# Performance work log

Measured on AMD Instinct MI355X. Metric: run time of the kernel, lower is better.

The kernel has to match this reference:

```python
import jax, jax.numpy as jnp
import numpy as np

# ---- static config (mirrors PaCoVoxelLoss init) ----
NUM_QUERIES = 20
FACTOR = 64
NUM_GT = 12
K_NEIGHBORS = 8          # repulsion.num_neighbors
REP_EPS = 1e-12          # repulsion.epsilon
BANDWIDTH = 0.03         # repulsion.kernel_bandwidth
RADIUS = 0.07            # repulsion.radius
ALPHA_PARAM = 0.5
BETA_CHAMFER = 20.0
W_CLS, W_REP, W_CH1, W_CH2 = 1.0, 1.0, 1.0, 1.0
PAD_COST = 1e6           # pad value to square the rectangular assignment problem


def _hungarian(cost):
    # Jonker-Volgenant / e-maxx shortest augmenting path; cost: (n, n) float64.
    # Returns col_to_row: for each column j, the row assigned to it.
    n = cost.shape[0]
    INF = 1e18
    u = np.zeros(n + 1); v = np.zeros(n + 1)
    p = np.zeros(n + 1, dtype=np.int64)
    way = np.zeros(n + 1, dtype=np.int64)
    for i in range(1, n + 1):
        p[0] = i; j0 = 0
        minv = np.full(n + 1, INF)
        used = np.zeros(n + 1, dtype=bool)
        while True:
            used[j0] = True
            i0 = p[j0]; delta = INF; j1 = 0
            for j in range(1, n + 1):
                if not used[j]:
                    cur = cost[i0 - 1, j - 1] - u[i0] - v[j]
                    if cur < minv[j]:
                        minv[j] = cur; way[j] = j0
                    if minv[j] < delta:
                        delta = minv[j]; j1 = j
            for j in range(n + 1):
                if used[j]:
                    u[p[j]] += delta; v[j] -= delta
                else:
                    minv[j] -= delta
            j0 = j1
            if p[j0] == 0:
                break
        while j0 != 0:
            j1 = way[j0]; p[j0] = p[j1]; j0 = j1
    return p[1:] - 1


def _match(cost_np):
    # cost_np: (B, Q, P) with P <= Q -> rows (B, P): pred row matched to each gt col.
    Bn, Qn, Pn = cost_np.shape
    rows = np.zeros((Bn, Pn), dtype=np.int64)
    for b in range(Bn):
        sq = np.full((Qn, Qn), PAD_COST, dtype=np.float64)
        sq[:, :Pn] = cost_np[b].astype(np.float64)
        rows[b] = _hungarian(sq)[:Pn]
    return rows


def _gather_q(A, rows):
    # A: (B, Q, P), rows: (B, P) -> A[b, rows[b,p], p] : (B, P)
    return jnp.take_along_axis(A, rows[:, None, :], axis=1)[:, 0, :]


def _bce_logits(x, t):
    return jnp.maximum(x, 0.0) - x * t + jnp.log1p(jnp.exp(-jnp.abs(x)))


def _cost_terms(pred_normals, pred_distances, gt_normals, gt_distances, points, gt_masks):
    mask_f = gt_masks.astype(points.dtype)           # (B, P, N)
    cnt = mask_f.sum(-1)                             # (B, P)
    # |points . n_q - d_q| for all query planes: (B, Q, N)
    pp = jnp.abs(jnp.einsum('bnd,bqd->bqn', points, pred_normals) - pred_distances[:, :, None])
    cham_raw = jnp.einsum('bqn,bpn->bqp', pp, mask_f) / jnp.maximum(cnt, 1.0)[:, None, :]
    has = (cnt > 0)[:, None, :]                      # (B, 1, P)
    normal_sim = 1.0 - jnp.abs(jnp.einsum('bqd,bpd->bqp', pred_normals, gt_normals))
    dist_diff = jnp.abs(pred_distances[:, :, None] - gt_distances[:, None, :])
    cost = normal_sim + 0.5 * dist_diff + 5.0 * jnp.where(has, cham_raw, 1.0)
    return cost, cham_raw, normal_sim, dist_diff, has


def _losses(pred_logits, pred_normals, pred_distances, gt_normals, gt_distances,
            points, reconstructed_points, gt, gt_masks, rows):
    _, cham_raw, normal_sim, dist_diff, has = _cost_terms(
        pred_normals, pred_distances, gt_normals, gt_distances, points, gt_masks)

    # classification loss: target 1 at matched pred rows
    Qn = pred_logits.shape[1]
    cls_target = jax.nn.one_hot(rows, Qn, dtype=pred_logits.dtype).sum(axis=1)  # (B, Q)
    cls_loss = _bce_logits(pred_logits, cls_target).mean()

    # param loss over matched pairs (mean over P matches, mean over B)
    param_loss = (_gather_q(normal_sim, rows).mean(-1) + _gather_q(dist_diff, rows).mean(-1)).mean()

    # pvd chamfer: point-to-plane term, zero for empty masks, /P /B
    pvd_chamfer = _gather_q(jnp.where(has, cham_raw, 0.0), rows).mean()

    # repulsion loss on per-query point groups
    Bn = reconstructed_points.shape[0]
    rp = reconstructed_points.reshape(Bn, NUM_QUERIES, FACTOR, 3)
    d2 = jnp.sum((rp[:, :, :, None, :] - rp[:, :, None, :, :]) ** 2, axis=-1)  # (B,Q,F,F)
    _, idx = jax.lax.top_k(-d2, K_NEIGHBORS)       # k nearest incl. self
    dn = jnp.maximum(jnp.take_along_axis(d2, idx[..., 1:], axis=-1), REP_EPS)  # (B,Q,F,k-1)
    w = jnp.exp(-dn / BANDWIDTH ** 2)
    rep = jnp.maximum(jnp.mean((RADIUS - jnp.sqrt(dn)) * w, axis=(2, 3)), 0.0).mean()

    # fine-grained chamfer (L1 and L2) between reconstructed and gt clouds
    diff = reconstructed_points[:, :, None, :] - gt[:, None, :, :]  # (B, M, G, 3)
    d1 = jnp.abs(diff).sum(-1)
    d2c = (diff ** 2).sum(-1)
    ch1 = (0.5 * (d1.min(axis=2).mean(axis=1) + d1.min(axis=1).mean(axis=1))).mean()
    ch2 = (0.5 * (d2c.min(axis=2).mean(axis=1) + d2c.min(axis=1).mean(axis=1))).mean()

    total = (W_CLS * cls_loss + ALPHA_PARAM * param_loss + BETA_CHAMFER * pvd_chamfer
             + W_REP * rep + W_CH1 * ch1 + W_CH2 * ch2)
    return total


def setup_inputs() -> dict:
    key = jax.random.key(0)
    ks = jax.random.split(key, 10)
    B, Q, P, N, G = 8, NUM_QUERIES, NUM_GT, 4096, 2048

    def unit(k, shape):
        v = jax.random.normal(k, shape, dtype=jnp.float32)
        return v / jnp.linalg.norm(v, axis=-1, keepdims=True)

    return {
        'pred_logits': jax.random.normal(ks[0], (B, Q), dtype=jnp.float32),
        'pred_normals': unit(ks[1], (B, Q, 3)),
        'pred_distances': jax.random.normal(ks[2], (B, Q), dtype=jnp.float32),
        'gt_normals': unit(ks[3], (B, P, 3)),
        'gt_distances': jax.random.normal(ks[4], (B, P), dtype=jnp.float32),
        'gt_masks': jax.random.bernoulli(ks[5], 0.3, (B, P, N)),
        'points': jax.random.normal(ks[6], (B, N, 3), dtype=jnp.float32),
        'reconstructed_points': 0.5 * jax.random.normal(ks[7], (B, Q * FACTOR, 3), dtype=jnp.float32),
        'gt': jax.random.normal(ks[8], (B, G, 3), dtype=jnp.float32),
        'gt_index': jax.random.randint(ks[9], (B, G), 0, P, dtype=jnp.int64) if jax.config.jax_enable_x64 else jax.random.randint(ks[9], (B, G), 0, P, dtype=jnp.int32),
    }


def reference(pred_logits, pred_normals, pred_distances, gt_normals, gt_distances,
              points, reconstructed_points, gt, gt_masks, gt_index):
    cost = _cost_terms(pred_normals, pred_distances, gt_normals, gt_distances, points, gt_masks)[0]
    rows = jnp.asarray(_match(np.asarray(cost)))  # Hungarian (host, like scipy in original)
    return _losses(pred_logits, pred_normals, pred_distances, gt_normals, gt_distances,
                   points, reconstructed_points, gt, gt_masks, rows)
```

## Files before the change

### kernel.cpp

```cpp
#include <hip/hip_runtime.h>
#include <math.h>

#define Bn 8
#define Qn 20
#define Pn 12
#define Nn 4096
#define Gn 2048
#define Mn 1280
#define Fn 64
#define KNB 7
#define SA 8
#define SB 5


__global__ void mega1_kernel(const float* __restrict__ pred_normals,
                             const float* __restrict__ pred_distances,
                             const float* __restrict__ gt_normals,
                             const float* __restrict__ gt_distances,
                             const float* __restrict__ points,
                             const int*   __restrict__ gt_masks,
                             const float* __restrict__ recon,
                             const float* __restrict__ gt,
                             float* __restrict__ cham, float* __restrict__ ns,
                             float* __restrict__ dd, float* __restrict__ cost,
                             float* __restrict__ cnt, float* __restrict__ acc,
                             float* __restrict__ rep_part,
                             float* __restrict__ pmA1, float* __restrict__ pmA2,
                             float* __restrict__ pmB1, float* __restrict__ pmB2) {
    __shared__ float smem[2 * Pn * 256];
    const int blk = blockIdx.x;
    const int tid = threadIdx.x;

    if (blk < 160) {
        if (blk == 0 && tid < 20) acc[tid] = 0.f;
        const int b = blk / Qn, q = blk % Qn;
        const float nx = pred_normals[(b * Qn + q) * 3 + 0];
        const float ny = pred_normals[(b * Qn + q) * 3 + 1];
        const float nz = pred_normals[(b * Qn + q) * 3 + 2];
        const float dq = pred_distances[b * Qn + q];

        float accs[Pn], accw[Pn];
#pragma unroll
        for (int p = 0; p < Pn; ++p) { accs[p] = 0.f; accw[p] = 0.f; }

        const float* ptb = points + (size_t)b * Nn * 3;
        const int*   mb  = gt_masks + (size_t)b * Pn * Nn;

        for (int n = tid; n < Nn; n += 256) {
            float px = ptb[n * 3 + 0], py = ptb[n * 3 + 1], pz = ptb[n * 3 + 2];
            float pp = fabsf(px * nx + py * ny + pz * nz - dq);
#pragma unroll
            for (int p = 0; p < Pn; ++p) {
                float m = (float)mb[(size_t)p * Nn + n];
                accs[p] += pp * m;
                accw[p] += m;
            }
        }
#pragma unroll
        for (int p = 0; p < Pn; ++p) {
            smem[p * 256 + tid] = accs[p];
            smem[(p + Pn) * 256 + tid] = accw[p];
        }
        __syncthreads();
        for (int off = 128; off > 0; off >>= 1) {
            if (tid < off) {
#pragma unroll
                for (int r = 0; r < 2 * Pn; ++r) smem[r * 256 + tid] += smem[r * 256 + tid + off];
            }
            __syncthreads();
        }
        if (tid < Pn) {
            const int p = tid;
            float c  = smem[(p + Pn) * 256];
            float cv = smem[p * 256] / fmaxf(c, 1.f);
            float gnx = gt_normals[(b * Pn + p) * 3 + 0];
            float gny = gt_normals[(b * Pn + p) * 3 + 1];
            float gnz = gt_normals[(b * Pn + p) * 3 + 2];
            float nsim = 1.f - fabsf(nx * gnx + ny * gny + nz * gnz);
            float ddv  = fabsf(dq - gt_distances[b * Pn + p]);
            int idx = (b * Qn + q) * Pn + p;
            cham[idx] = cv;
            ns[idx]   = nsim;
            dd[idx]   = ddv;
            cost[idx] = nsim + 0.5f * ddv + 5.f * ((c > 0.f) ? cv : 1.f);
            if (q == 0) cnt[b * Pn + p] = c;
        }
    } else if (blk < 200) {
        const int wave = tid >> 6, lane = tid & 63;
        const int g = (blk - 160) * 4 + wave;
        float* xs = smem + wave * 192;
        float* ys = xs + 64;
        float* zs = xs + 128;
        const float* base = recon + (size_t)g * Fn * 3;
        xs[lane] = base[lane * 3 + 0];
        ys[lane] = base[lane * 3 + 1];
        zs[lane] = base[lane * 3 + 2];
        __syncthreads();
        float best[KNB];
#pragma unroll
        for (int k = 0; k < KNB; ++k) best[k] = 3.4e38f;
        const float xi = xs[lane], yi = ys[lane], zi = zs[lane];
        for (int j = 0; j < Fn; ++j) {
            if (j == lane) continue;
            float dx = xi - xs[j], dy = yi - ys[j], dz = zi - zs[j];
            float d2 = dx * dx + dy * dy + dz * dz;
            if (d2 < best[KNB - 1]) {
                int k = KNB - 1;
                while (k > 0 && best[k - 1] > d2) { best[k] = best[k - 1]; --k; }
                best[k] = d2;
            }
        }
        float sum = 0.f;
#pragma unroll
        for (int k = 0; k < KNB; ++k) {
            float dn = fmaxf(best[k], 1e-12f);
            float w  = expf(-dn / (0.03f * 0.03f));
            sum += (0.07f - sqrtf(dn)) * w;
        }
        for (int off = 32; off > 0; off >>= 1) sum += __shfl_down(sum, off);
        if (lane == 0) rep_part[g] = fmaxf(sum / (float)(Fn * KNB), 0.f);
    } else {
        int cblk = blk - 200;
        float* tx = smem;
        float* ty = smem + 256;
        float* tz = smem + 512;
        float x, y, z;
        const float* inner;
        float *o1, *o2;
        int idx;
        if (cblk < 40 * SA) {
            int s = cblk % SA, ob = cblk / SA;
            idx = ob * 256 + tid;
            int b = idx / Mn;
            x = recon[idx * 3 + 0]; y = recon[idx * 3 + 1]; z = recon[idx * 3 + 2];
            inner = gt + ((size_t)b * Gn + s * 256) * 3;
            o1 = pmA1 + s * (Bn * Mn); o2 = pmA2 + s * (Bn * Mn);
        } else {
            cblk -= 40 * SA;
            int s = cblk % SB, ob = cblk / SB;
            idx = ob * 256 + tid;
            int b = idx / Gn;
            x = gt[idx * 3 + 0]; y = gt[idx * 3 + 1]; z = gt[idx * 3 + 2];
            inner = recon + ((size_t)b * Mn + s * 256) * 3;
            o1 = pmB1 + s * (Bn * Gn); o2 = pmB2 + s * (Bn * Gn);
        }
        tx[tid] = inner[tid * 3 + 0];
        ty[tid] = inner[tid * 3 + 1];
        tz[tid] = inner[tid * 3 + 2];
        __syncthreads();
        float m1 = 3.4e38f, m2 = 3.4e38f;
        for (int j = 0; j < 256; ++j) {
            float dx = x - tx[j], dy = y - ty[j], dz = z - tz[j];
            float d1 = fabsf(dx) + fabsf(dy) + fabsf(dz);
            float d2 = dx * dx + dy * dy + dz * dz;
            m1 = fminf(m1, d1); m2 = fminf(m2, d2);
        }
        o1[idx] = m1; o2[idx] = m2;
    }
}

__global__ void hungarian_kernel(const float* __restrict__ cost,
                                 const float* __restrict__ pred_logits,
                                 const float* __restrict__ ns,
                                 const float* __restrict__ dd,
                                 const float* __restrict__ cham,
                                 const float* __restrict__ cnt,
                                 float* __restrict__ acc) {
    const int b = blockIdx.x;
    const int t = threadIdx.x;
    __shared__ double a[Pn * Qn];
    for (int k = t; k < Qn * Pn; k += 64)
        a[(k % Pn) * Qn + (k / Pn)] = (double)cost[b * Qn * Pn + k];
    __syncthreads();

    const int col = t;
    const bool isCol = (col >= 1 && col <= Qn);
    double v = 0.0;
    double u = 0.0;
    double minv = 0.0;
    int way = 0, p = 0;

    for (int i = 1; i <= Pn; ++i) {
        const int p0 = i;
        minv = 1e18;
        bool used = false;
        bool rowInPath = false;
        int j0 = 0;
        while (true) {
            if (col == j0) used = true;
            int i0 = (j0 == 0) ? p0 : __shfl(p, j0);
            if (t == i0) rowInPath = true;
            double u_i0 = __shfl(u, i0);
            double mv = 1e18;
            if (isCol && !used) {
                double cur = a[(i0 - 1) * Qn + (col - 1)] - u_i0 - v;
                if (cur < minv) { minv = cur; way = j0; }
                mv = minv;
            }
            double bv = mv; int bj = col;
#pragma unroll
            for (int off = 16; off > 0; off >>= 1) {
                double ov = __shfl_down(bv, off);
                int    oj = __shfl_down(bj, off);
                if (ov < bv) { bv = ov; bj = oj; }
            }
            double delta = __shfl(bv, 0);
            int    j1    = __shfl(bj, 0);
            if (used || col == 0) v -= delta;
            else if (isCol)       minv -= delta;
            if (rowInPath)        u += delta;
            j0 = j1;
            int pj0 = __shfl(p, j0);
            if (pj0 == 0) break;
        }
        while (j0 != 0) {
            int wj = __shfl(way, j0);
            int pw = (wj == 0) ? p0 : __shfl(p, wj);
            if (col == j0) p = pw;
            j0 = wj;
        }
    }

    float cls = 0.f, par = 0.f, pvd = 0.f;
    if (isCol) {
        float x = pred_logits[b * Qn + (col - 1)];
        float tgt = (p > 0) ? 1.f : 0.f;
        cls = fmaxf(x, 0.f) - x * tgt + log1pf(expf(-fabsf(x)));
        if (p > 0) {
            int idx = (b * Qn + (col - 1)) * Pn + (p - 1);
            par = ns[idx] + dd[idx];
            pvd = (cnt[b * Pn + (p - 1)] > 0.f) ? cham[idx] : 0.f;
        }
    }
    for (int off = 32; off > 0; off >>= 1) {
        cls += __shfl_down(cls, off);
        par += __shfl_down(par, off);
        pvd += __shfl_down(pvd, off);
    }
    if (t == 0) {
        atomicAdd(&acc[0], cls / (float)(Bn * Qn));
        atomicAdd(&acc[1], par / (float)(Bn * Pn));
        atomicAdd(&acc[2], pvd / (float)(Bn * Pn));
    }
}

__global__ void reduce_kernel(const float* __restrict__ pmA1, const float* __restrict__ pmA2,
                              const float* __restrict__ pmB1, const float* __restrict__ pmB2,
                              const float* __restrict__ rep_part,
                              float* __restrict__ acc, int* __restrict__ counter,
                              float* __restrict__ out) {
    const int blk = blockIdx.x;
    const int tid = threadIdx.x;
    float c1 = 0.f, c2 = 0.f;
    if (blk < 40) {
        int idx = blk * 256 + tid;
        float m1 = 3.4e38f, m2 = 3.4e38f;
#pragma unroll
        for (int s = 0; s < SA; ++s) {
            m1 = fminf(m1, pmA1[s * (Bn * Mn) + idx]);
            m2 = fminf(m2, pmA2[s * (Bn * Mn) + idx]);
        }
        c1 = m1 * (0.5f / (float)(Bn * Mn));
        c2 = m2 * (0.5f / (float)(Bn * Mn));
    } else if (blk < 104) {
        int idx = (blk - 40) * 256 + tid;
        float m1 = 3.4e38f, m2 = 3.4e38f;
#pragma unroll
        for (int s = 0; s < SB; ++s) {
            m1 = fminf(m1, pmB1[s * (Bn * Gn) + idx]);
            m2 = fminf(m2, pmB2[s * (Bn * Gn) + idx]);
        }
        c1 = m1 * (0.5f / (float)(Bn * Gn));
        c2 = m2 * (0.5f / (float)(Bn * Gn));
    } else {
        c1 = (tid < Bn * Qn) ? rep_part[tid] / (float)(Bn * Qn) : 0.f;
    }
    __shared__ float s1[256], s2[256];
    s1[tid] = c1; s2[tid] = c2;
    __syncthreads();
    for (int off = 128; off > 0; off >>= 1) {
        if (tid < off) { s1[tid] += s1[tid + off]; s2[tid] += s2[tid + off]; }
        __syncthreads();
    }
    if (tid == 0) {
        if (blk < 104) {
            atomicAdd(&acc[4], s1[0]);
            atomicAdd(&acc[5], s2[0]);
        } else {
            atomicAdd(&acc[3], s1[0]);
        }
        __threadfence();
        int old = atomicAdd(counter, 1);
        if (old == 104) {
            float a0 = atomicAdd(&acc[0], 0.f);
            float a1 = atomicAdd(&acc[1], 0.f);
            float a2 = atomicAdd(&acc[2], 0.f);
            float a3 = atomicAdd(&acc[3], 0.f);
            float a4 = atomicAdd(&acc[4], 0.f);
            float a5 = atomicAdd(&acc[5], 0.f);
            out[0] = a0 + 0.5f * a1 + 20.f * a2 + a3 + a4 + a5;
        }
    }
}

extern "C" void kernel_launch(void* const* d_in, const int* in_sizes, int n_in,
                              void* d_out, int out_size, void* d_ws, size_t ws_size,
                              hipStream_t stream) {
    const float* pred_logits    = (const float*)d_in[0];
    const float* pred_normals   = (const float*)d_in[1];
    const float* pred_distances = (const float*)d_in[2];
    const float* gt_normals     = (const float*)d_in[3];
    const float* gt_distances   = (const float*)d_in[4];
    const int*   gt_masks       = (const int*)d_in[5];
    const float* points         = (const float*)d_in[6];
    const float* recon          = (const float*)d_in[7];
    const float* gt             = (const float*)d_in[8];

    float* ws   = (float*)d_ws;
    float* cham = ws;
    float* ns   = ws + 1920;
    float* dd   = ws + 3840;
    float* cost = ws + 5760;
    float* cnt  = ws + 7680;
    float* acc  = ws + 7872;
    int*   cntr = (int*)(ws + 7888);
    float* rep  = ws + 7904;
    float* pmA1 = ws + 8192;
    float* pmA2 = ws + 90112;
    float* pmB1 = ws + 172032;
    float* pmB2 = ws + 253952;

    mega1_kernel<<<840, 256, 0, stream>>>(pred_normals, pred_distances, gt_normals,
                                          gt_distances, points, gt_masks, recon, gt,
                                          cham, ns, dd, cost, cnt, acc, rep,
                                          pmA1, pmA2, pmB1, pmB2);
    hungarian_kernel<<<Bn, 64, 0, stream>>>(cost, pred_logits, ns, dd, cham, cnt, acc);
    reduce_kernel<<<105, 256, 0, stream>>>(pmA1, pmA2, pmB1, pmB2, rep, acc, cntr,
                                           (float*)d_out);
}
```

Before: 135.4 us.

## Fuse Hungarian and chamfer reduction into main kernel via last-block completion counters

Merges the Hungarian matching kernel and the final reduce kernel into one kernel, adding a small init kernel that zeroes the counters and fills the min buffers with +inf. The last of the 20 cost blocks for each batch runs the Hungarian match. Chamfer partial minima now go through atomicMin on float bits instead of per-slice buffers, and the last slice block for each tile reduces the tile. A global done counter picks which block writes the final output. This removes kernel launch boundaries and intermediate buffer traffic, at the price of atomic writes, counter serialization and a tail that is still serialized.

```diff
diff --git a/kernel.cpp b/kernel.cpp
--- a/kernel.cpp
+++ b/kernel.cpp
@@ -11,28 +11,66 @@
 #define KNB 7
 #define SA 8
 #define SB 5
-
-
-__global__ void mega1_kernel(const float* __restrict__ pred_normals,
-                             const float* __restrict__ pred_distances,
-                             const float* __restrict__ gt_normals,
-                             const float* __restrict__ gt_distances,
-                             const float* __restrict__ points,
-                             const int*   __restrict__ gt_masks,
-                             const float* __restrict__ recon,
-                             const float* __restrict__ gt,
-                             float* __restrict__ cham, float* __restrict__ ns,
-                             float* __restrict__ dd, float* __restrict__ cost,
-                             float* __restrict__ cnt, float* __restrict__ acc,
-                             float* __restrict__ rep_part,
-                             float* __restrict__ pmA1, float* __restrict__ pmA2,
-                             float* __restrict__ pmB1, float* __restrict__ pmB2) {
+#define DONE_TARGET 152
+
+
+__device__ __forceinline__ float aread(float* p) { return atomicAdd(p, 0.0f); }
+__device__ __forceinline__ void awrite(float* p, float v) { atomicExch(p, v); }
+__device__ __forceinline__ unsigned int auread(unsigned int* p) { return atomicAdd(p, 0u); }
+
+__device__ __forceinline__ void contribute(float* acc, int* done, float* out) {
+    __threadfence();
+    int old = atomicAdd(done, 1);
+    if (old == DONE_TARGET - 1) {
+        __threadfence();
+        float a0 = aread(&acc[0]);
+        float a1 = aread(&acc[1]);
+        float a2 = aread(&acc[2]);
+        float a3 = aread(&acc[3]);
+        float a4 = aread(&acc[4]);
+        float a5 = aread(&acc[5]);
+        out[0] = a0 + 0.5f * a1 + 20.f * a2 + a3 + a4 + a5;
+    }
+}
+
+__global__ void init_kernel(unsigned int* wsu) {
+    int tid = blockIdx.x * 256 + threadIdx.x;
+    for (int k = tid; k < 160; k += 64 * 256) wsu[7776 + k] = 0u;
+    for (int k = tid; k < 53248; k += 64 * 256) wsu[8192 + k] = 0x7F800000u;
+}
+
+__global__ void mega_kernel(const float* __restrict__ pred_logits,
+                            const float* __restrict__ pred_normals,
+                            const float* __restrict__ pred_distances,
+                            const float* __restrict__ gt_normals,
+                            const float* __restrict__ gt_distances,
+                            const float* __restrict__ points,
+                            const int*   __restrict__ gt_masks,
+                            const float* __restrict__ recon,
+                            const float* __restrict__ gt,
+                            float* __restrict__ ws, float* __restrict__ out) {
     __shared__ float smem[2 * Pn * 256];
+    __shared__ double hsm[Pn * Qn];
+    __shared__ int sflag;
     const int blk = blockIdx.x;
     const int tid = threadIdx.x;
 
+    float* cham = ws;
+    float* ns   = ws + 1920;
+    float* dd   = ws + 3840;
+    float* cost = ws + 5760;
+    float* cnt  = ws + 7680;
+    float* acc  = ws + 7776;
+    int*   costc  = (int*)(ws + 7784);
+    int*   chamAc = (int*)(ws + 7792);
+    int*   chamBc = (int*)(ws + 7832);
+    int*   done   = (int*)(ws + 7896);
+    unsigned int* mA1u = (unsigned int*)(ws + 8192);
+    unsigned int* mA2u = (unsigned int*)(ws + 18432);
+    unsigned int* mB1u = (unsigned int*)(ws + 28672);
+    unsigned int* mB2u = (unsigned int*)(ws + 45056);
+
     if (blk < 160) {
-        if (blk == 0 && tid < 20) acc[tid] = 0.f;
         const int b = blk / Qn, q = blk % Qn;
         const float nx = pred_normals[(b * Qn + q) * 3 + 0];
         const float ny = pred_normals[(b * Qn + q) * 3 + 1];
@@ -79,11 +117,94 @@
             float nsim = 1.f - fabsf(nx * gnx + ny * gny + nz * gnz);
             float ddv  = fabsf(dq - gt_distances[b * Pn + p]);
             int idx = (b * Qn + q) * Pn + p;
-            cham[idx] = cv;
-            ns[idx]   = nsim;
-            dd[idx]   = ddv;
-            cost[idx] = nsim + 0.5f * ddv + 5.f * ((c > 0.f) ? cv : 1.f);
-            if (q == 0) cnt[b * Pn + p] = c;
+            awrite(&cham[idx], cv);
+            awrite(&ns[idx],   nsim);
+            awrite(&dd[idx],   ddv);
+            awrite(&cost[idx], nsim + 0.5f * ddv + 5.f * ((c > 0.f) ? cv : 1.f));
+            if (q == 0) awrite(&cnt[b * Pn + p], c);
+        }
+        __syncthreads();
+        if (tid == 0) {
+            __threadfence();
+            int old = atomicAdd(&costc[b], 1);
+            sflag = (old == Qn - 1) ? 1 : 0;
+        }
+        __syncthreads();
+        if (!sflag) return;
+        if (tid >= 64) return;
+        __threadfence();
+
+        const int t = tid;
+        for (int k = t; k < Qn * Pn; k += 64)
+            hsm[(k % Pn) * Qn + (k / Pn)] = (double)aread(&cost[b * Qn * Pn + k]);
+
+        const int col = t;
+        const bool isCol = (col >= 1 && col <= Qn);
+        double v = 0.0, u = 0.0, minv = 0.0;
+        int way = 0, p = 0;
+
+        for (int i = 1; i <= Pn; ++i) {
+            const int p0 = i;
+            minv = 1e18;
+            bool used = false;
+            bool rowInPath = false;
+            int j0 = 0;
+            while (true) {
+                if (col == j0) used = true;
+                int i0 = (j0 == 0) ? p0 : __shfl(p, j0);
+                if (t == i0) rowInPath = true;
+                double u_i0 = __shfl(u, i0);
+                double mv = 1e18;
+                if (isCol && !used) {
+                    double cur = hsm[(i0 - 1) * Qn + (col - 1)] - u_i0 - v;
+                    if (cur < minv) { minv = cur; way = j0; }
+                    mv = minv;
+                }
+                double bv = mv; int bj = col;
+#pragma unroll
+                for (int off = 16; off > 0; off >>= 1) {
+                    double ov = __shfl_down(bv, off);
+                    int    oj = __shfl_down(bj, off);
+                    if (ov < bv) { bv = ov; bj = oj; }
+                }
+                double delta = __shfl(bv, 0);
+                int    j1    = __shfl(bj, 0);
+                if (used || col == 0) v -= delta;
+                else if (isCol)       minv -= delta;
+                if (rowInPath)        u += delta;
+                j0 = j1;
+                int pj0 = __shfl(p, j0);
+                if (pj0 == 0) break;
+            }
+            while (j0 != 0) {
+                int wj = __shfl(way, j0);
+                int pw = (wj == 0) ? p0 : __shfl(p, wj);
+                if (col == j0) p = pw;
+                j0 = wj;
+            }
+        }
+
+        float cls = 0.f, par = 0.f, pvd = 0.f;
+        if (isCol) {
+            float x = pred_logits[b * Qn + (col - 1)];
+            float tgt = (p > 0) ? 1.f : 0.f;
+            cls = fmaxf(x, 0.f) - x * tgt + log1pf(expf(-fabsf(x)));
+            if (p > 0) {
+                int idx = (b * Qn + (col - 1)) * Pn + (p - 1);
+                par = aread(&ns[idx]) + aread(&dd[idx]);
+                pvd = (aread(&cnt[b * Pn + (p - 1)]) > 0.f) ? aread(&cham[idx]) : 0.f;
+            }
+        }
+        for (int off = 32; off > 0; off >>= 1) {
+            cls += __shfl_down(cls, off);
+            par += __shfl_down(par, off);
+            pvd += __shfl_down(pvd, off);
+        }
+        if (t == 0) {
+            atomicAdd(&acc[0], cls / (float)(Bn * Qn));
+            atomicAdd(&acc[1], par / (float)(Bn * Pn));
+            atomicAdd(&acc[2], pvd / (float)(Bn * Pn));
+            contribute(acc, done, out);
         }
     } else if (blk < 200) {
         const int wave = tid >> 6, lane = tid & 63;
@@ -95,7 +216,6 @@
         xs[lane] = base[lane * 3 + 0];
         ys[lane] = base[lane * 3 + 1];
         zs[lane] = base[lane * 3 + 2];
-        __syncthreads();
         float best[KNB];
 #pragma unroll
         for (int k = 0; k < KNB; ++k) best[k] = 3.4e38f;
@@ -118,32 +238,40 @@
             sum += (0.07f - sqrtf(dn)) * w;
         }
         for (int off = 32; off > 0; off >>= 1) sum += __shfl_down(sum, off);
-        if (lane == 0) rep_part[g] = fmaxf(sum / (float)(Fn * KNB), 0.f);
+        if (lane == 0) smem[1000 + wave] = fmaxf(sum / (float)(Fn * KNB), 0.f);
+        __syncthreads();
+        if (tid == 0) {
+            float total = (smem[1000] + smem[1001] + smem[1002] + smem[1003]) / (float)(Bn * Qn);
+            atomicAdd(&acc[3], total);
+            contribute(acc, done, out);
+        }
     } else {
-        int cblk = blk - 200;
-        float* tx = smem;
-        float* ty = smem + 256;
-        float* tz = smem + 512;
+        int a = blk - 200;
+        const bool isA = (a < 320);
+        int ob, s, idx;
         float x, y, z;
         const float* inner;
-        float *o1, *o2;
-        int idx;
-        if (cblk < 40 * SA) {
-            int s = cblk % SA, ob = cblk / SA;
+        unsigned int *mu1, *mu2;
+        int* ctr; int target;
+        if (isA) {
+            ob = a / SA; s = a % SA;
             idx = ob * 256 + tid;
             int b = idx / Mn;
             x = recon[idx * 3 + 0]; y = recon[idx * 3 + 1]; z = recon[idx * 3 + 2];
             inner = gt + ((size_t)b * Gn + s * 256) * 3;
-            o1 = pmA1 + s * (Bn * Mn); o2 = pmA2 + s * (Bn * Mn);
+            mu1 = mA1u; mu2 = mA2u; ctr = &chamAc[ob]; target = SA;
         } else {
-            cblk -= 40 * SA;
-            int s = cblk % SB, ob = cblk / SB;
+            a -= 320;
+            ob = a / SB; s = a % SB;
             idx = ob * 256 + tid;
             int b = idx / Gn;
             x = gt[idx * 3 + 0]; y = gt[idx * 3 + 1]; z = gt[idx * 3 + 2];
             inner = recon + ((size_t)b * Mn + s * 256) * 3;
-            o1 = pmB1 + s * (Bn * Gn); o2 = pmB2 + s * (Bn * Gn);
-        }
+            mu1 = mB1u; mu2 = mB2u; ctr = &chamBc[ob]; target = SB;
+        }
+        float* tx = smem;
+        float* ty = smem + 256;
+        float* tz = smem + 512;
         tx[tid] = inner[tid * 3 + 0];
         ty[tid] = inner[tid * 3 + 1];
         tz[tid] = inner[tid * 3 + 2];
@@ -155,150 +283,33 @@
             float d2 = dx * dx + dy * dy + dz * dz;
             m1 = fminf(m1, d1); m2 = fminf(m2, d2);
         }
-        o1[idx] = m1; o2[idx] = m2;
-    }
-}
-
-__global__ void hungarian_kernel(const float* __restrict__ cost,
-                                 const float* __restrict__ pred_logits,
-                                 const float* __restrict__ ns,
-                                 const float* __restrict__ dd,
-                                 const float* __restrict__ cham,
-                                 const float* __restrict__ cnt,
-                                 float* __restrict__ acc) {
-    const int b = blockIdx.x;
-    const int t = threadIdx.x;
-    __shared__ double a[Pn * Qn];
-    for (int k = t; k < Qn * Pn; k += 64)
-        a[(k % Pn) * Qn + (k / Pn)] = (double)cost[b * Qn * Pn + k];
-    __syncthreads();
-
-    const int col = t;
-    const bool isCol = (col >= 1 && col <= Qn);
-    double v = 0.0;
-    double u = 0.0;
-    double minv = 0.0;
-    int way = 0, p = 0;
-
-    for (int i = 1; i <= Pn; ++i) {
-        const int p0 = i;
-        minv = 1e18;
-        bool used = false;
-        bool rowInPath = false;
-        int j0 = 0;
-        while (true) {
-            if (col == j0) used = true;
-            int i0 = (j0 == 0) ? p0 : __shfl(p, j0);
-            if (t == i0) rowInPath = true;
-            double u_i0 = __shfl(u, i0);
-            double mv = 1e18;
-            if (isCol && !used) {
-                double cur = a[(i0 - 1) * Qn + (col - 1)] - u_i0 - v;
-                if (cur < minv) { minv = cur; way = j0; }
-                mv = minv;
-            }
-            double bv = mv; int bj = col;
-#pragma unroll
-            for (int off = 16; off > 0; off >>= 1) {
-                double ov = __shfl_down(bv, off);
-                int    oj = __shfl_down(bj, off);
-                if (ov < bv) { bv = ov; bj = oj; }
-            }
-            double delta = __shfl(bv, 0);
-            int    j1    = __shfl(bj, 0);
-            if (used || col == 0) v -= delta;
-            else if (isCol)       minv -= delta;
-            if (rowInPath)        u += delta;
-            j0 = j1;
-            int pj0 = __shfl(p, j0);
-            if (pj0 == 0) break;
-        }
-        while (j0 != 0) {
-            int wj = __shfl(way, j0);
-            int pw = (wj == 0) ? p0 : __shfl(p, wj);
-            if (col == j0) p = pw;
-            j0 = wj;
-        }
-    }
-
-    float cls = 0.f, par = 0.f, pvd = 0.f;
-    if (isCol) {
-        float x = pred_logits[b * Qn + (col - 1)];
-        float tgt = (p > 0) ? 1.f : 0.f;
-        cls = fmaxf(x, 0.f) - x * tgt + log1pf(expf(-fabsf(x)));
-        if (p > 0) {
-            int idx = (b * Qn + (col - 1)) * Pn + (p - 1);
-            par = ns[idx] + dd[idx];
-            pvd = (cnt[b * Pn + (p - 1)] > 0.f) ? cham[idx] : 0.f;
-        }
-    }
-    for (int off = 32; off > 0; off >>= 1) {
-        cls += __shfl_down(cls, off);
-        par += __shfl_down(par, off);
-        pvd += __shfl_down(pvd, off);
-    }
-    if (t == 0) {
-        atomicAdd(&acc[0], cls / (float)(Bn * Qn));
-        atomicAdd(&acc[1], par / (float)(Bn * Pn));
-        atomicAdd(&acc[2], pvd / (float)(Bn * Pn));
-    }
-}
-
-__global__ void reduce_kernel(const float* __restrict__ pmA1, const float* __restrict__ pmA2,
-                              const float* __restrict__ pmB1, const float* __restrict__ pmB2,
-                              const float* __restrict__ rep_part,
-                              float* __restrict__ acc, int* __restrict__ counter,
-                              float* __restrict__ out) {
-    const int blk = blockIdx.x;
-    const int tid = threadIdx.x;
-    float c1 = 0.f, c2 = 0.f;
-    if (blk < 40) {
-        int idx = blk * 256 + tid;
-        float m1 = 3.4e38f, m2 = 3.4e38f;
-#pragma unroll
-        for (int s = 0; s < SA; ++s) {
-            m1 = fminf(m1, pmA1[s * (Bn * Mn) + idx]);
-            m2 = fminf(m2, pmA2[s * (Bn * Mn) + idx]);
-        }
-        c1 = m1 * (0.5f / (float)(Bn * Mn));
-        c2 = m2 * (0.5f / (float)(Bn * Mn));
-    } else if (blk < 104) {
-        int idx = (blk - 40) * 256 + tid;
-        float m1 = 3.4e38f, m2 = 3.4e38f;
-#pragma unroll
-        for (int s = 0; s < SB; ++s) {
-            m1 = fminf(m1, pmB1[s * (Bn * Gn) + idx]);
-            m2 = fminf(m2, pmB2[s * (Bn * Gn) + idx]);
-        }
-        c1 = m1 * (0.5f / (float)(Bn * Gn));
-        c2 = m2 * (0.5f / (float)(Bn * Gn));
-    } else {
-        c1 = (tid < Bn * Qn) ? rep_part[tid] / (float)(Bn * Qn) : 0.f;
-    }
-    __shared__ float s1[256], s2[256];
-    s1[tid] = c1; s2[tid] = c2;
-    __syncthreads();
-    for (int off = 128; off > 0; off >>= 1) {
-        if (tid < off) { s1[tid] += s1[tid + off]; s2[tid] += s2[tid + off]; }
-        __syncthreads();
-    }
-    if (tid == 0) {
-        if (blk < 104) {
+        atomicMin(&mu1[idx], __float_as_uint(m1));
+        atomicMin(&mu2[idx], __float_as_uint(m2));
+        __syncthreads();
+        if (tid == 0) {
+            __threadfence();
+            int old = atomicAdd(ctr, 1);
+            sflag = (old == target - 1) ? 1 : 0;
+        }
+        __syncthreads();
+        if (!sflag) return;
+        __threadfence();
+        float scale = isA ? (0.5f / (float)(Bn * Mn)) : (0.5f / (float)(Bn * Gn));
+        float c1 = __uint_as_float(auread(&mu1[idx])) * scale;
+        float c2 = __uint_as_float(auread(&mu2[idx])) * scale;
+        float* s1 = smem;
+        float* s2 = smem + 256;
+        __syncthreads();
+        s1[tid] = c1; s2[tid] = c2;
+        __syncthreads();
+        for (int off = 128; off > 0; off >>= 1) {
+            if (tid < off) { s1[tid] += s1[tid + off]; s2[tid] += s2[tid + off]; }
+            __syncthreads();
+        }
+        if (tid == 0) {
             atomicAdd(&acc[4], s1[0]);
             atomicAdd(&acc[5], s2[0]);
-        } else {
-            atomicAdd(&acc[3], s1[0]);
-        }
-        __threadfence();
-        int old = atomicAdd(counter, 1);
-        if (old == 104) {
-            float a0 = atomicAdd(&acc[0], 0.f);
-            float a1 = atomicAdd(&acc[1], 0.f);
-            float a2 = atomicAdd(&acc[2], 0.f);
-            float a3 = atomicAdd(&acc[3], 0.f);
-            float a4 = atomicAdd(&acc[4], 0.f);
-            float a5 = atomicAdd(&acc[5], 0.f);
-            out[0] = a0 + 0.5f * a1 + 20.f * a2 + a3 + a4 + a5;
+            contribute(acc, done, out);
         }
     }
 }
@@ -316,25 +327,8 @@
     const float* recon          = (const float*)d_in[7];
     const float* gt             = (const float*)d_in[8];
 
-    float* ws   = (float*)d_ws;
-    float* cham = ws;
-    float* ns   = ws + 1920;
-    float* dd   = ws + 3840;
-    float* cost = ws + 5760;
-    float* cnt  = ws + 7680;
-    float* acc  = ws + 7872;
-    int*   cntr = (int*)(ws + 7888);
-    float* rep  = ws + 7904;
-    float* pmA1 = ws + 8192;
-    float* pmA2 = ws + 90112;
-    float* pmB1 = ws + 172032;
-    float* pmB2 = ws + 253952;
-
-    mega1_kernel<<<840, 256, 0, stream>>>(pred_normals, pred_distances, gt_normals,
-                                          gt_distances, points, gt_masks, recon, gt,
-                                          cham, ns, dd, cost, cnt, acc, rep,
-                                          pmA1, pmA2, pmB1, pmB2);
-    hungarian_kernel<<<Bn, 64, 0, stream>>>(cost, pred_logits, ns, dd, cham, cnt, acc);
-    reduce_kernel<<<105, 256, 0, stream>>>(pmA1, pmA2, pmB1, pmB2, rep, acc, cntr,
-                                           (float*)d_out);
+    init_kernel<<<64, 256, 0, stream>>>((unsigned int*)d_ws);
+    mega_kernel<<<840, 256, 0, stream>>>(pred_logits, pred_normals, pred_distances,
+                                         gt_normals, gt_distances, points, gt_masks,
+                                         recon, gt, (float*)d_ws, (float*)d_out);
 }
```

After: 147.6 us. 1.09x slower.
